# Kernel tuning notes

Measured on AMD Instinct MI355X. Metric: run time of the kernel, lower is better.

## Reference

```python
import jax, jax.numpy as jnp
import numpy as np

B, N, D, A = 256, 32, 128, 16
DOA, E, FD, H, O = 144, 128, 128, 256, 1  # obs_act_in, obs_out/embed, final_in, hidden, final_out


def setup_inputs() -> dict:
    key = jax.random.key(0)
    ks = jax.random.split(key, 12)
    p = lambda k, shape: jax.random.normal(k, shape, jnp.float32) * 0.05
    return {
        "states": jax.random.normal(ks[0], (B, N, D), jnp.float32),
        "policies": jax.random.uniform(ks[1], (B, N, A), dtype=jnp.float32),
        "actions": jax.random.uniform(ks[2], (B, N, A), dtype=jnp.float32),
        "Wk_proc": p(ks[3], (D, E)),
        "Wq_proc": p(ks[4], (D, E)),
        "Wv_proc": p(ks[5], (D, E)),
        "Wk": p(ks[6], (E, FD)),
        "Wq": p(ks[7], (E, FD)),
        "We": p(ks[8], (DOA, E)),
        "Wav": p(ks[9], (E, FD)),
        "W1": p(ks[10], (FD, H)),
        "W2": p(ks[11], (H, O)),
    }


def reference(states, policies, actions, Wk_proc, Wq_proc, Wv_proc, Wk, Wq, We, Wav, W1, W2):
    n = states.shape[1]
    # NOTE: original code divides BOTH attention stages by sqrt(self.d_k_obs) = final_input_dim
    scale = 1.0 / jnp.sqrt(jnp.asarray(Wk.shape[1], states.dtype))

    # stage-1 attention over agents [B,N,N]
    k1 = states @ Wk_proc
    q1 = states @ Wq_proc
    v1 = states @ Wv_proc
    w1 = jax.nn.softmax(jnp.einsum('bie,bje->bij', q1, k1) * scale, axis=-1)
    wav1 = jnp.einsum('bij,bje->bie', w1, v1)  # [B,N,E]

    # stage-2 attention weights
    k2 = wav1 @ Wk
    q2 = wav1 @ Wq
    w2 = jax.nn.softmax(jnp.einsum('bif,bjf->bij', q2, k2) * scale, axis=-1)

    # build obs-action/policy tensor: entry [b,i,j] uses policy of agent j when i==j else action of j
    oa = jnp.concatenate([states, actions], axis=-1)   # [B,N,DOA]
    op = jnp.concatenate([states, policies], axis=-1)  # [B,N,DOA]
    eye = jnp.eye(n, dtype=states.dtype)[:, :, None]   # [N,N,1]
    oap = eye * op[:, None, :, :] + (1.0 - eye) * oa[:, None, :, :]  # [B,N,N,DOA]

    av = (oap @ We) @ Wav  # [B,N,N,FD]

    # node_features[b,i,j,f] = sum_k w2[b,i,k] * av[b,j,k,f]  (avoids the 5D repeat)
    node = jnp.einsum('bik,bjkf->bijf', w2, av)

    h = node @ W1
    h = jnp.where(h > 0, h, 0.01 * h)  # leaky_relu, default slope
    value = h @ W2  # [B,N,N,O]
    return value, w1, w2
```

## Files before the change

### kernel.cpp

```cpp
#include <hip/hip_runtime.h>
#include <math.h>

#define NB 256
#define NN 32
#define DD 128
#define NA 16
#define HH 256

using f32x4v  = __attribute__((ext_vector_type(4))) float;
using bf16x8  = __attribute__((ext_vector_type(8))) short;

static __device__ __forceinline__ float4 ld4(const float* p){ return *reinterpret_cast<const float4*>(p); }
static __device__ __forceinline__ void st4f(float* p, float4 v){ *reinterpret_cast<float4*>(p) = v; }
static __device__ __forceinline__ float elem(float4 v, int kk){
    return (kk==0)?v.x:(kk==1)?v.y:(kk==2)?v.z:v.w;
}

static __device__ __forceinline__ unsigned f2bf(float x){
    unsigned u = __float_as_uint(x);
    u += 0x7fffu + ((u >> 16) & 1u);
    return u >> 16;
}
static __device__ __forceinline__ unsigned pack2(float a, float b){
    return f2bf(a) | (f2bf(b) << 16);
}
static __device__ __forceinline__ float bf2f(unsigned short s){
    return __uint_as_float(((unsigned)s) << 16);
}

static __device__ __forceinline__ f32x4v mfma16(bf16x8 a, bf16x8 b, f32x4v c){
    return __builtin_amdgcn_mfma_f32_16x16x32_bf16(a, b, c, 0, 0, 0);
}

static __device__ __forceinline__ bf16x8 to_bf8(const float v[8]){
    union { bf16x8 v8; unsigned u[4]; } r;
    #pragma unroll
    for (int j = 0; j < 4; j++) r.u[j] = pack2(v[2*j], v[2*j+1]);
    return r.v8;
}

static __device__ __forceinline__ void store_frag(unsigned short* __restrict__ dst,
                                                  int frag, int l, const float v[8]){
    uint4 p;
    p.x = pack2(v[0], v[1]); p.y = pack2(v[2], v[3]);
    p.z = pack2(v[4], v[5]); p.w = pack2(v[6], v[7]);
    *reinterpret_cast<uint4*>(dst + (size_t)(frag*64 + l)*8) = p;
}

__global__ __launch_bounds__(512)
void k_pre(const float* __restrict__ We, const float* __restrict__ Wav,
           const float* __restrict__ W1,
           const float* __restrict__ Wqp, const float* __restrict__ Wkp,
           const float* __restrict__ Wvp, const float* __restrict__ Wq,
           const float* __restrict__ Wk,
           float* __restrict__ WABf, unsigned short* __restrict__ WABs,
           unsigned short* __restrict__ Wqps, unsigned short* __restrict__ Wkps,
           unsigned short* __restrict__ Wvps, unsigned short* __restrict__ Wqs,
           unsigned short* __restrict__ Wks)
{
    const int t = threadIdx.x;
    const int bid = blockIdx.x;

    if (bid < 16) {
        __shared__ float T2f[128*20];
        __shared__ float WABt[160*16];
        const int ct = bid;
        const int l  = t & 63, wvv = t >> 6;
        const int lg = l >> 4;
        const int lc = l & 15;

        {
            const int arow = wvv*16 + lc;
            f32x4v acc = {0.f,0.f,0.f,0.f};
            #pragma unroll
            for (int kt = 0; kt < 4; kt++) {
                const float* ap = Wav + (size_t)arow*128 + kt*32 + lg*8;
                float4 a0 = ld4(ap), a1 = ld4(ap + 4);
                float av8[8] = {a0.x,a0.y,a0.z,a0.w,a1.x,a1.y,a1.z,a1.w};
                const float* bp = W1 + (size_t)(kt*32 + lg*8)*256 + ct*16 + lc;
                float bv8[8];
                #pragma unroll
                for (int i = 0; i < 8; i++) bv8[i] = bp[(size_t)i*256];
                acc = mfma16(to_bf8(av8), to_bf8(bv8), acc);
            }
            const int dr = wvv*16 + lg*4;
            #pragma unroll
            for (int r = 0; r < 4; r++) T2f[(dr+r)*20 + lc] = acc[r];
        }
        __syncthreads();

        #pragma unroll
        for (int pass = 0; pass < 2; pass++) {
            const int mt = (pass == 0) ? wvv : 8 + wvv;
            if (pass == 1 && wvv >= 2) continue;
            const int arow = mt*16 + lc;
            f32x4v acc = {0.f,0.f,0.f,0.f};
            #pragma unroll
            for (int kt = 0; kt < 4; kt++) {
                float av8[8];
                if (arow < 144) {
                    const float* ap = We + (size_t)arow*128 + kt*32 + lg*8;
                    float4 a0 = ld4(ap), a1 = ld4(ap + 4);
                    av8[0]=a0.x; av8[1]=a0.y; av8[2]=a0.z; av8[3]=a0.w;
                    av8[4]=a1.x; av8[5]=a1.y; av8[6]=a1.z; av8[7]=a1.w;
                } else {
                    #pragma unroll
                    for (int i = 0; i < 8; i++) av8[i] = 0.f;
                }
                float bv8[8];
                #pragma unroll
                for (int i = 0; i < 8; i++) bv8[i] = T2f[(kt*32 + lg*8 + i)*20 + lc];
                acc = mfma16(to_bf8(av8), to_bf8(bv8), acc);
            }
            const int dr = mt*16 + lg*4;
            #pragma unroll
            for (int r = 0; r < 4; r++) WABt[(dr+r)*16 + lc] = acc[r];
            if (mt == 8) {
                #pragma unroll
                for (int r = 0; r < 4; r++)
                    WABf[(size_t)(dr+r)*256 + ct*16 + lc] = acc[r];
            }
        }
        __syncthreads();

        if (t < 320) {
            int kt = t >> 6, ll = t & 63;
            float v[8];
            #pragma unroll
            for (int i = 0; i < 8; i++)
                v[i] = WABt[(kt*32 + (ll>>4)*8 + i)*16 + (ll&15)];
            store_frag(WABs, kt*16 + ct, ll, v);
        }
    } else {
        const int bb = bid - 16;
        const int fg = bb*8 + (t >> 6);
        const int l  = t & 63;
        const int sel = fg >> 5, frag = fg & 31;
        const int kt = frag >> 3, nt = frag & 7;
        const float* W = (sel==0) ? Wqp : (sel==1) ? Wkp : (sel==2) ? Wvp :
                         (sel==3) ? Wq : Wk;
        unsigned short* dst = (sel==0) ? Wqps : (sel==1) ? Wkps : (sel==2) ? Wvps :
                              (sel==3) ? Wqs : Wks;
        float v[8];
        #pragma unroll
        for (int i = 0; i < 8; i++)
            v[i] = W[(kt*32 + (l>>4)*8 + i)*128 + nt*16 + (l&15)];
        store_frag(dst, frag, l, v);
    }
}

static __device__ __forceinline__ void scores_softmax512(const float* __restrict__ Qm,
                                                         const float* __restrict__ Km,
                                                         float scale,
                                                         float* __restrict__ w_lds,
                                                         float* __restrict__ w_out,
                                                         int i, int j)
{
    float s0 = 0.f, s1 = 0.f;
    #pragma unroll 4
    for (int k=0;k<128;k+=4){
        float4 qv = ld4(Qm + i*132 + k);
        float4 k0 = ld4(Km + j*132 + k);
        float4 k1 = ld4(Km + (j+16)*132 + k);
        s0 += qv.x*k0.x + qv.y*k0.y + qv.z*k0.z + qv.w*k0.w;
        s1 += qv.x*k1.x + qv.y*k1.y + qv.z*k1.z + qv.w*k1.w;
    }
    s0 *= scale; s1 *= scale;
    float m = fmaxf(s0, s1);
    #pragma unroll
    for (int d=1; d<16; d<<=1) m = fmaxf(m, __shfl_xor(m, d));
    float e0 = expf(s0 - m), e1 = expf(s1 - m);
    float sum = e0 + e1;
    #pragma unroll
    for (int d=1; d<16; d<<=1) sum += __shfl_xor(sum, d);
    float inv = 1.f / sum;
    e0 *= inv; e1 *= inv;
    w_lds[i*36 + j]      = e0;
    w_lds[i*36 + j + 16] = e1;
    w_out[i*32 + j]      = e0;
    w_out[i*32 + j + 16] = e1;
}

__global__ __launch_bounds__(512)
void k_main(const float* __restrict__ states, const float* __restrict__ pol,
            const float* __restrict__ act,
            const unsigned short* __restrict__ Wqps, const unsigned short* __restrict__ Wkps,
            const unsigned short* __restrict__ Wvps, const unsigned short* __restrict__ Wqs,
            const unsigned short* __restrict__ Wks,  const unsigned short* __restrict__ WABs,
            const float* __restrict__ WABf, const float* __restrict__ W2,
            float* __restrict__ out_v, float* __restrict__ out_w1,
            float* __restrict__ out_w2)
{
    const int b = blockIdx.x;
    const int t = threadIdx.x;
    const float scale = 0.08838834764831845f;

    __shared__ float SH[16000];
    float* B1   = SH;
    float* B2   = SH + 4224;
    float* Wb2f = SH + 8448;
    float* Wb1f = SH + 9600;
    float* APd  = SH + 10752;
    unsigned short* Xoa  = (unsigned short*)(SH + 11264);
    unsigned short* Ubf  = (unsigned short*)B1;
    unsigned short* Wvbf = (unsigned short*)B2;
    float*    A1 = SH;
    unsigned* P2 = (unsigned*)(SH + 11904);
    unsigned* Q2 = (unsigned*)SH;
    float* SPQ = Wb1f;

    const float* stg  = states + (size_t)b*(NN*DD);
    const float* actg = act + (size_t)b*(NN*NA);
    const float* polg = pol + (size_t)b*(NN*NA);

    {
        int r = t >> 4, kb = t & 15;
        #pragma unroll
        for (int uu = 0; uu < 10; uu++){
            int k = kb + 16*uu;
            float v = (k < 128) ? stg[r*128 + k]
                    : (k < 144) ? actg[r*16 + (k-128)] : 0.f;
            Xoa[r*168 + k] = (unsigned short)f2bf(v);
        }
        if (t < 128) {
            int rr = t>>2, cc = (t&3)*4;
            float4 p = ld4(polg + rr*16 + cc), a = ld4(actg + rr*16 + cc);
            st4f(APd + rr*16 + cc, make_float4(p.x-a.x, p.y-a.y, p.z-a.z, p.w-a.w));
        }
    }
    __syncthreads();

    const int l    = t & 63;
    const int wv   = t >> 6;
    const int mt   = wv & 1;
    const int ntb  = (wv >> 1) * 2;
    const int nb7  = (wv >> 1) * 4;
    const int arow = mt*16 + (l & 15);
    const int drow = mt*16 + ((l >> 4) << 2);
    const int dcol = l & 15;

    const int c  = t & 127;
    const int g  = t >> 7;
    const int cp = (t & 127)*2;
    const int si = t >> 4;
    const int sj = t & 15;
    const int wp = wv & 1;

    {
        f32x4v aq0={0.f,0.f,0.f,0.f}, aq1={0.f,0.f,0.f,0.f};
        f32x4v ak0={0.f,0.f,0.f,0.f}, ak1={0.f,0.f,0.f,0.f};
        const unsigned short* ab = Xoa + arow*168 + (l>>4)*8;
        #pragma unroll
        for (int kt = 0; kt < 4; kt++){
            bf16x8 a   = *reinterpret_cast<const bf16x8*>(ab + kt*32);
            bf16x8 bq0 = *reinterpret_cast<const bf16x8*>(Wqps + (size_t)((kt*8+ntb  )*64 + l)*8);
            bf16x8 bq1 = *reinterpret_cast<const bf16x8*>(Wqps + (size_t)((kt*8+ntb+1)*64 + l)*8);
            bf16x8 bk0 = *reinterpret_cast<const bf16x8*>(Wkps + (size_t)((kt*8+ntb  )*64 + l)*8);
            bf16x8 bk1 = *reinterpret_cast<const bf16x8*>(Wkps + (size_t)((kt*8+ntb+1)*64 + l)*8);
            aq0 = mfma16(a, bq0, aq0); aq1 = mfma16(a, bq1, aq1);
            ak0 = mfma16(a, bk0, ak0); ak1 = mfma16(a, bk1, ak1);
        }
        #pragma unroll
        for (int r = 0; r < 4; r++){
            B1[(drow+r)*132 + ntb*16     + dcol] = aq0[r];
            B1[(drow+r)*132 + (ntb+1)*16 + dcol] = aq1[r];
            B2[(drow+r)*132 + ntb*16     + dcol] = ak0[r];
            B2[(drow+r)*132 + (ntb+1)*16 + dcol] = ak1[r];
        }
    }
    __syncthreads();

    scores_softmax512(B1, B2, scale, Wb1f, out_w1 + (size_t)b*1024, si, sj);
    __syncthreads();

    {
        float au[8];
        #pragma unroll
        for (int u=0;u<8;u++) au[u]=0.f;
        #pragma unroll
        for (int k0=0;k0<32;k0+=4){
            float4 xv[8];
            #pragma unroll
            for (int u=0;u<8;u++) xv[u] = ld4(Wb1f + (g*8+u)*36 + k0);
            #pragma unroll
            for (int kk=0;kk<4;kk++){
                float w = bf2f(Xoa[(k0+kk)*168 + c]);
                #pragma unroll
                for (int u=0;u<8;u++) au[u] = fmaf(elem(xv[u],kk), w, au[u]);
            }
        }
        __syncthreads();
        #pragma unroll
        for (int u=0;u<8;u++) Ubf[(g*8+u)*136 + c] = (unsigned short)f2bf(au[u]);
    }
    __syncthreads();

    {
        f32x4v av0={0.f,0.f,0.f,0.f}, av1={0.f,0.f,0.f,0.f};
        const unsigned short* ab = Ubf + arow*136 + (l>>4)*8;
        #pragma unroll
        for (int kt = 0; kt < 4; kt++){
            bf16x8 a  = *reinterpret_cast<const bf16x8*>(ab + kt*32);
            bf16x8 b0 = *reinterpret_cast<const bf16x8*>(Wvps + (size_t)((kt*8+ntb  )*64 + l)*8);
            bf16x8 b1 = *reinterpret_cast<const bf16x8*>(Wvps + (size_t)((kt*8+ntb+1)*64 + l)*8);
            av0 = mfma16(a, b0, av0); av1 = mfma16(a, b1, av1);
        }
        #pragma unroll
        for (int r = 0; r < 4; r++){
            Wvbf[(drow+r)*136 + ntb*16     + dcol] = (unsigned short)f2bf(av0[r]);
            Wvbf[(drow+r)*136 + (ntb+1)*16 + dcol] = (unsigned short)f2bf(av1[r]);
        }
    }
    __syncthreads();

    {
        f32x4v aq0={0.f,0.f,0.f,0.f}, aq1={0.f,0.f,0.f,0.f};
        f32x4v ak0={0.f,0.f,0.f,0.f}, ak1={0.f,0.f,0.f,0.f};
        const unsigned short* ab = Wvbf + arow*136 + (l>>4)*8;
        #pragma unroll
        for (int kt = 0; kt < 4; kt++){
            bf16x8 a   = *reinterpret_cast<const bf16x8*>(ab + kt*32);
            bf16x8 bq0 = *reinterpret_cast<const bf16x8*>(Wqs + (size_t)((kt*8+ntb  )*64 + l)*8);
            bf16x8 bq1 = *reinterpret_cast<const bf16x8*>(Wqs + (size_t)((kt*8+ntb+1)*64 + l)*8);
            bf16x8 bk0 = *reinterpret_cast<const bf16x8*>(Wks + (size_t)((kt*8+ntb  )*64 + l)*8);
            bf16x8 bk1 = *reinterpret_cast<const bf16x8*>(Wks + (size_t)((kt*8+ntb+1)*64 + l)*8);
            aq0 = mfma16(a, bq0, aq0); aq1 = mfma16(a, bq1, aq1);
            ak0 = mfma16(a, bk0, ak0); ak1 = mfma16(a, bk1, ak1);
        }
        __syncthreads();
        #pragma unroll
        for (int r = 0; r < 4; r++){
            B1[(drow+r)*132 + ntb*16     + dcol] = aq0[r];
            B1[(drow+r)*132 + (ntb+1)*16 + dcol] = aq1[r];
            B2[(drow+r)*132 + ntb*16     + dcol] = ak0[r];
            B2[(drow+r)*132 + (ntb+1)*16 + dcol] = ak1[r];
        }
    }
    __syncthreads();

    scores_softmax512(B1, B2, scale, Wb2f, out_w2 + (size_t)b*1024, si, sj);
    __syncthreads();

    {
        f32x4v ac[4];
        #pragma unroll
        for (int n=0;n<4;n++) ac[n] = f32x4v{0.f,0.f,0.f,0.f};
        const unsigned short* ab = Xoa + arow*168 + (l>>4)*8;
        #pragma unroll
        for (int kt = 0; kt < 5; kt++){
            bf16x8 a = *reinterpret_cast<const bf16x8*>(ab + kt*32);
            #pragma unroll
            for (int n = 0; n < 4; n++){
                bf16x8 bb = *reinterpret_cast<const bf16x8*>(WABs + (size_t)((kt*16 + nb7 + n)*64 + l)*8);
                ac[n] = mfma16(a, bb, ac[n]);
            }
        }
        #pragma unroll
        for (int n = 0; n < 4; n++){
            #pragma unroll
            for (int r = 0; r < 4; r++)
                A1[(drow+r)*260 + (nb7+n)*16 + dcol] = ac[n][r];
        }
    }
    __syncthreads();

    {
        float ap0[8], ap1[8];
        #pragma unroll
        for (int u=0;u<8;u++){ ap0[u]=0.f; ap1[u]=0.f; }
        #pragma unroll
        for (int k0=0;k0<32;k0+=4){
            float4 xv[8];
            #pragma unroll
            for (int u=0;u<8;u++) xv[u] = ld4(Wb2f + (g*8+u)*36 + k0);
            #pragma unroll
            for (int kk=0;kk<4;kk++){
                float2 w = *reinterpret_cast<const float2*>(A1 + (k0+kk)*260 + cp);
                #pragma unroll
                for (int u=0;u<8;u++){
                    float x = elem(xv[u],kk);
                    ap0[u] = fmaf(x, w.x, ap0[u]);
                    ap1[u] = fmaf(x, w.y, ap1[u]);
                }
            }
        }
        __syncthreads();
        #pragma unroll
        for (int u=0;u<8;u++)
            P2[(g*8+u)*128 + (cp>>1)] = pack2(ap0[u], ap1[u]);
        float2 w2v = *reinterpret_cast<const float2*>(W2 + cp);
        float sp[8];
        #pragma unroll
        for (int u=0;u<8;u++) sp[u] = ap0[u]*w2v.x + ap1[u]*w2v.y;
        #pragma unroll
        for (int d=1; d<64; d<<=1){
            #pragma unroll
            for (int u=0;u<8;u++) sp[u] += __shfl_xor(sp[u], d);
        }
        if (l == 0){
            #pragma unroll
            for (int u=0;u<8;u++) SPQ[(g*8+u)*2 + wp] = sp[u];
        }
    }
    __syncthreads();

    {
        float aq0[8], aq1[8];
        #pragma unroll
        for (int u=0;u<8;u++){ aq0[u]=0.f; aq1[u]=0.f; }
        const float* wB = WABf + 128*256;
        #pragma unroll
        for (int k0=0;k0<16;k0+=4){
            float4 xv[8];
            #pragma unroll
            for (int u=0;u<8;u++) xv[u] = ld4(APd + (g*8+u)*16 + k0);
            #pragma unroll
            for (int kk=0;kk<4;kk++){
                float2 w = *reinterpret_cast<const float2*>(wB + (k0+kk)*256 + cp);
                #pragma unroll
                for (int u=0;u<8;u++){
                    float x = elem(xv[u],kk);
                    aq0[u] = fmaf(x, w.x, aq0[u]);
                    aq1[u] = fmaf(x, w.y, aq1[u]);
                }
            }
        }
        #pragma unroll
        for (int u=0;u<8;u++)
            Q2[(g*8+u)*132 + (cp>>1)] = pack2(aq0[u], aq1[u]);
        float2 w2v = *reinterpret_cast<const float2*>(W2 + cp);
        float sq[8];
        #pragma unroll
        for (int u=0;u<8;u++) sq[u] = aq0[u]*w2v.x + aq1[u]*w2v.y;
        #pragma unroll
        for (int d=1; d<64; d<<=1){
            #pragma unroll
            for (int u=0;u<8;u++) sq[u] += __shfl_xor(sq[u], d);
        }
        if (l == 0){
            #pragma unroll
            for (int u=0;u<8;u++) SPQ[64 + (g*8+u)*2 + wp] = sq[u];
        }
    }
    __syncthreads();

    {
        float w00 = Wb2f[si*36 + sj], w01 = Wb2f[si*36 + sj + 16];
        float SPi = SPQ[si*2] + SPQ[si*2+1];
        float SQa = SPQ[64 + sj*2] + SPQ[64 + sj*2+1];
        float SQb = SPQ[64 + (sj+16)*2] + SPQ[64 + (sj+16)*2+1];
        float a0 = 0.f, a1 = 0.f;

        #define PROC(PA,QA,QB,H2) {                                         \
            float w2e = W2[(H2)], w2o = W2[(H2)+1];                         \
            float paE = __uint_as_float((PA)<<16), paO = __uint_as_float((PA) & 0xffff0000u); \
            float qaE = __uint_as_float((QA)<<16), qaO = __uint_as_float((QA) & 0xffff0000u); \
            float qbE = __uint_as_float((QB)<<16), qbO = __uint_as_float((QB) & 0xffff0000u); \
            float t0 = fmaf(w00, qaE, paE); a0 = fmaf(fabsf(t0), w2e, a0);  \
            float t1 = fmaf(w00, qaO, paO); a0 = fmaf(fabsf(t1), w2o, a0);  \
            float t2 = fmaf(w01, qbE, paE); a1 = fmaf(fabsf(t2), w2e, a1);  \
            float t3 = fmaf(w01, qbO, paO); a1 = fmaf(fabsf(t3), w2o, a1); }

        #pragma unroll 4
        for (int hp4 = 0; hp4 < 32; hp4++){
            uint4 pa4 = *reinterpret_cast<const uint4*>(P2 + si*128 + hp4*4);
            uint4 qa4 = *reinterpret_cast<const uint4*>(Q2 + sj*132 + hp4*4);
            uint4 qb4 = *reinterpret_cast<const uint4*>(Q2 + (sj+16)*132 + hp4*4);
            PROC(pa4.x, qa4.x, qb4.x, hp4*8+0)
            PROC(pa4.y, qa4.y, qb4.y, hp4*8+2)
            PROC(pa4.z, qa4.z, qb4.z, hp4*8+4)
            PROC(pa4.w, qa4.w, qb4.w, hp4*8+6)
        }
        #undef PROC

        float* ov = out_v + (size_t)b*1024;
        ov[si*32 + sj]      = fmaf(0.495f, a0, 0.505f*(SPi + w00*SQa));
        ov[si*32 + sj + 16] = fmaf(0.495f, a1, 0.505f*(SPi + w01*SQb));
    }
}

extern "C" void kernel_launch(void* const* d_in, const int* in_sizes, int n_in,
                              void* d_out, int out_size, void* d_ws, size_t ws_size,
                              hipStream_t stream) {
    const float* states = (const float*)d_in[0];
    const float* pol    = (const float*)d_in[1];
    const float* act    = (const float*)d_in[2];
    const float* Wkp    = (const float*)d_in[3];
    const float* Wqp    = (const float*)d_in[4];
    const float* Wvp    = (const float*)d_in[5];
    const float* Wk     = (const float*)d_in[6];
    const float* Wq     = (const float*)d_in[7];
    const float* We     = (const float*)d_in[8];
    const float* Wav    = (const float*)d_in[9];
    const float* W1     = (const float*)d_in[10];
    const float* W2     = (const float*)d_in[11];

    float* out    = (float*)d_out;
    float* out_v  = out;
    float* out_w1 = out + 256*1024;
    float* out_w2 = out + 2*256*1024;

    float* WABf = (float*)d_ws;
    unsigned short* WABs = (unsigned short*)(WABf + 36864);
    unsigned short* wsu  = (unsigned short*)(WABf + 57344);
    unsigned short* Wqps = wsu;
    unsigned short* Wkps = wsu + 16384;
    unsigned short* Wvps = wsu + 32768;
    unsigned short* Wqs  = wsu + 49152;
    unsigned short* Wks  = wsu + 65536;

    hipLaunchKernelGGL(k_pre, dim3(36), dim3(512), 0, stream,
                       We, Wav, W1, Wqp, Wkp, Wvp, Wq, Wk,
                       WABf, WABs, Wqps, Wkps, Wvps, Wqs, Wks);
    hipLaunchKernelGGL(k_main, dim3(NB), dim3(512), 0, stream,
                       states, pol, act,
                       Wqps, Wkps, Wvps, Wqs, Wks, WABs, WABf, W2,
                       out_v, out_w1, out_w2);
}
```

Baseline: 39.10 us.

## Fuse weight-prep and main kernels into one cooperative launch with grid sync

Merges the weight preprocessing kernel and the per-batch main kernel into a single cooperative kernel. The first 36 blocks do the weight repacking, then all 256 blocks pass a grid-wide barrier before the per-batch work. The goal is to remove the second kernel launch and the inter-kernel gap. In exchange it adds a grid sync, and the cooperative launch requires all 256 blocks of 512 threads to be co-resident.

Result: slower. 120.9 us (+209.2%).

```diff
diff --git a/kernel.cpp b/kernel.cpp
--- a/kernel.cpp
+++ b/kernel.cpp
@@ -1,5 +1,8 @@
 #include <hip/hip_runtime.h>
+#include <hip/hip_cooperative_groups.h>
 #include <math.h>
+
+namespace cg = cooperative_groups;
 
 #define NB 256
 #define NN 32
@@ -47,23 +50,60 @@
     *reinterpret_cast<uint4*>(dst + (size_t)(frag*64 + l)*8) = p;
 }
 
+static __device__ __forceinline__ void scores_softmax512(const float* __restrict__ Qm,
+                                                         const float* __restrict__ Km,
+                                                         float scale,
+                                                         float* __restrict__ w_lds,
+                                                         float* __restrict__ w_out,
+                                                         int i, int j)
+{
+    float s0 = 0.f, s1 = 0.f;
+    #pragma unroll 4
+    for (int k=0;k<128;k+=4){
+        float4 qv = ld4(Qm + i*132 + k);
+        float4 k0 = ld4(Km + j*132 + k);
+        float4 k1 = ld4(Km + (j+16)*132 + k);
+        s0 += qv.x*k0.x + qv.y*k0.y + qv.z*k0.z + qv.w*k0.w;
+        s1 += qv.x*k1.x + qv.y*k1.y + qv.z*k1.z + qv.w*k1.w;
+    }
+    s0 *= scale; s1 *= scale;
+    float m = fmaxf(s0, s1);
+    #pragma unroll
+    for (int d=1; d<16; d<<=1) m = fmaxf(m, __shfl_xor(m, d));
+    float e0 = expf(s0 - m), e1 = expf(s1 - m);
+    float sum = e0 + e1;
+    #pragma unroll
+    for (int d=1; d<16; d<<=1) sum += __shfl_xor(sum, d);
+    float inv = 1.f / sum;
+    e0 *= inv; e1 *= inv;
+    w_lds[i*36 + j]      = e0;
+    w_lds[i*36 + j + 16] = e1;
+    w_out[i*32 + j]      = e0;
+    w_out[i*32 + j + 16] = e1;
+}
+
 __global__ __launch_bounds__(512)
-void k_pre(const float* __restrict__ We, const float* __restrict__ Wav,
-           const float* __restrict__ W1,
-           const float* __restrict__ Wqp, const float* __restrict__ Wkp,
-           const float* __restrict__ Wvp, const float* __restrict__ Wq,
-           const float* __restrict__ Wk,
-           float* __restrict__ WABf, unsigned short* __restrict__ WABs,
-           unsigned short* __restrict__ Wqps, unsigned short* __restrict__ Wkps,
-           unsigned short* __restrict__ Wvps, unsigned short* __restrict__ Wqs,
-           unsigned short* __restrict__ Wks)
+void k_fused(const float* __restrict__ states, const float* __restrict__ pol,
+             const float* __restrict__ act,
+             const float* __restrict__ Wkp, const float* __restrict__ Wqp,
+             const float* __restrict__ Wvp, const float* __restrict__ Wk,
+             const float* __restrict__ Wq,  const float* __restrict__ We,
+             const float* __restrict__ Wav, const float* __restrict__ W1,
+             const float* __restrict__ W2,
+             float* __restrict__ out_v, float* __restrict__ out_w1,
+             float* __restrict__ out_w2,
+             float* __restrict__ WABf, unsigned short* __restrict__ WABs,
+             unsigned short* __restrict__ Wqps, unsigned short* __restrict__ Wkps,
+             unsigned short* __restrict__ Wvps, unsigned short* __restrict__ Wqs,
+             unsigned short* __restrict__ Wks)
 {
+    __shared__ float SH[16000];
     const int t = threadIdx.x;
     const int bid = blockIdx.x;
 
     if (bid < 16) {
-        __shared__ float T2f[128*20];
-        __shared__ float WABt[160*16];
+        float* T2f  = SH;
+        float* WABt = SH + 2560;
         const int ct = bid;
         const int l  = t & 63, wvv = t >> 6;
         const int lg = l >> 4;
@@ -131,7 +171,7 @@
                 v[i] = WABt[(kt*32 + (ll>>4)*8 + i)*16 + (ll&15)];
             store_frag(WABs, kt*16 + ct, ll, v);
         }
-    } else {
+    } else if (bid < 36) {
         const int bb = bid - 16;
         const int fg = bb*8 + (t >> 6);
         const int l  = t & 63;
@@ -147,55 +187,13 @@
             v[i] = W[(kt*32 + (l>>4)*8 + i)*128 + nt*16 + (l&15)];
         store_frag(dst, frag, l, v);
     }
-}
-
-static __device__ __forceinline__ void scores_softmax512(const float* __restrict__ Qm,
-                                                         const float* __restrict__ Km,
-                                                         float scale,
-                                                         float* __restrict__ w_lds,
-                                                         float* __restrict__ w_out,
-                                                         int i, int j)
-{
-    float s0 = 0.f, s1 = 0.f;
-    #pragma unroll 4
-    for (int k=0;k<128;k+=4){
-        float4 qv = ld4(Qm + i*132 + k);
-        float4 k0 = ld4(Km + j*132 + k);
-        float4 k1 = ld4(Km + (j+16)*132 + k);
-        s0 += qv.x*k0.x + qv.y*k0.y + qv.z*k0.z + qv.w*k0.w;
-        s1 += qv.x*k1.x + qv.y*k1.y + qv.z*k1.z + qv.w*k1.w;
-    }
-    s0 *= scale; s1 *= scale;
-    float m = fmaxf(s0, s1);
-    #pragma unroll
-    for (int d=1; d<16; d<<=1) m = fmaxf(m, __shfl_xor(m, d));
-    float e0 = expf(s0 - m), e1 = expf(s1 - m);
-    float sum = e0 + e1;
-    #pragma unroll
-    for (int d=1; d<16; d<<=1) sum += __shfl_xor(sum, d);
-    float inv = 1.f / sum;
-    e0 *= inv; e1 *= inv;
-    w_lds[i*36 + j]      = e0;
-    w_lds[i*36 + j + 16] = e1;
-    w_out[i*32 + j]      = e0;
-    w_out[i*32 + j + 16] = e1;
-}
-
-__global__ __launch_bounds__(512)
-void k_main(const float* __restrict__ states, const float* __restrict__ pol,
-            const float* __restrict__ act,
-            const unsigned short* __restrict__ Wqps, const unsigned short* __restrict__ Wkps,
-            const unsigned short* __restrict__ Wvps, const unsigned short* __restrict__ Wqs,
-            const unsigned short* __restrict__ Wks,  const unsigned short* __restrict__ WABs,
-            const float* __restrict__ WABf, const float* __restrict__ W2,
-            float* __restrict__ out_v, float* __restrict__ out_w1,
-            float* __restrict__ out_w2)
-{
-    const int b = blockIdx.x;
-    const int t = threadIdx.x;
+
+    __threadfence();
+    cg::this_grid().sync();
+
+    const int b = bid;
     const float scale = 0.08838834764831845f;
 
-    __shared__ float SH[16000];
     float* B1   = SH;
     float* B2   = SH + 4224;
     float* Wb2f = SH + 8448;
@@ -509,11 +507,14 @@
     unsigned short* Wqs  = wsu + 49152;
     unsigned short* Wks  = wsu + 65536;
 
-    hipLaunchKernelGGL(k_pre, dim3(36), dim3(512), 0, stream,
-                       We, Wav, W1, Wqp, Wkp, Wvp, Wq, Wk,
-                       WABf, WABs, Wqps, Wkps, Wvps, Wqs, Wks);
-    hipLaunchKernelGGL(k_main, dim3(NB), dim3(512), 0, stream,
-                       states, pol, act,
-                       Wqps, Wkps, Wvps, Wqs, Wks, WABs, WABf, W2,
-                       out_v, out_w1, out_w2);
-}
+    void* kargs[] = {
+        (void*)&states, (void*)&pol, (void*)&act,
+        (void*)&Wkp, (void*)&Wqp, (void*)&Wvp, (void*)&Wk, (void*)&Wq,
+        (void*)&We, (void*)&Wav, (void*)&W1, (void*)&W2,
+        (void*)&out_v, (void*)&out_w1, (void*)&out_w2,
+        (void*)&WABf, (void*)&WABs,
+        (void*)&Wqps, (void*)&Wkps, (void*)&Wvps, (void*)&Wqs, (void*)&Wks
+    };
+    hipLaunchCooperativeKernel((const void*)k_fused, dim3(NB), dim3(512),
+                               kargs, 0, stream);
+}
```
